# Kernel optimization log

Measured on AMD Instinct MI355X. Metric: run time of the kernel, lower is better.

## Reference

```python
import jax, jax.numpy as jnp
import numpy as np

N = 50000
E = 1600000
D_IN, H1, H2, N_CLS = 512, 128, 64, 10


def _add_self_loops(edge_index, n, edge_attr=None):
    loops = jnp.arange(n, dtype=edge_index.dtype)
    ei = jnp.concatenate([edge_index, jnp.stack([loops, loops])], axis=1)
    if edge_attr is None:
        return ei, None
    # PyG fill_value='mean' for self-loop edge attributes
    loop_attr = jnp.broadcast_to(jnp.mean(edge_attr, axis=0, keepdims=True), (n, edge_attr.shape[1]))
    return ei, jnp.concatenate([edge_attr, loop_attr], axis=0)


def _gat_conv(x, src, dst, n, W, a_src, a_dst, bias, edge_attr=None, We=None, a_edge=None):
    # single-head GATConv
    h = x @ W                                   # (N, out)
    alpha = (h * a_src).sum(-1)[src] + (h * a_dst).sum(-1)[dst]  # (E,)
    if edge_attr is not None:
        alpha = alpha + ((edge_attr @ We) * a_edge).sum(-1)
    alpha = jax.nn.leaky_relu(alpha, 0.2)
    # segment softmax over incoming edges of each dst node
    m = jax.ops.segment_max(alpha, dst, num_segments=n)
    e = jnp.exp(alpha - m[dst])
    s = jax.ops.segment_sum(e, dst, num_segments=n)
    coef = e / (s[dst] + 1e-16)
    out = jax.ops.segment_sum(h[src] * coef[:, None], dst, num_segments=n)
    return out + bias


def _prelu(x, a):
    return jnp.where(x >= 0, x, a * x)


def setup_inputs() -> dict:
    key = jax.random.key(0)
    ks = jax.random.split(key, 24)
    g = lambda k, shape, scale: (jax.random.normal(k, shape, dtype=jnp.float32) * scale)
    inp = {
        "x": jax.random.normal(ks[0], (N, D_IN), dtype=jnp.float32),
        "edge_index": jax.random.randint(ks[1], (2, E), 0, N, dtype=jnp.int32),
        "ppmi_edge_index": jax.random.randint(ks[2], (2, E), 0, N, dtype=jnp.int32),
        "ppmi_edge_attr": jax.random.uniform(ks[3], (E, 1), dtype=jnp.float32),
        # adjacency-branch GAT params
        "W1": g(ks[4], (D_IN, H1), (1.0 / D_IN) ** 0.5),
        "att_src1": g(ks[5], (H1,), 0.1), "att_dst1": g(ks[6], (H1,), 0.1),
        "b1": jnp.zeros((H1,), jnp.float32),
        "W2": g(ks[7], (H1, H2), (1.0 / H1) ** 0.5),
        "att_src2": g(ks[8], (H2,), 0.1), "att_dst2": g(ks[9], (H2,), 0.1),
        "b2": jnp.zeros((H2,), jnp.float32),
        "prelu_a": jnp.float32(0.25),
        # ppmi-branch GAT params (with edge_dim=1)
        "pW1": g(ks[10], (D_IN, H1), (1.0 / D_IN) ** 0.5),
        "patt_src1": g(ks[11], (H1,), 0.1), "patt_dst1": g(ks[12], (H1,), 0.1),
        "pWe1": g(ks[13], (1, H1), 1.0), "patt_e1": g(ks[14], (H1,), 0.1),
        "pb1": jnp.zeros((H1,), jnp.float32),
        "pW2": g(ks[15], (H1, H2), (1.0 / H1) ** 0.5),
        "patt_src2": g(ks[16], (H2,), 0.1), "patt_dst2": g(ks[17], (H2,), 0.1),
        "pWe2": g(ks[18], (1, H2), 1.0), "patt_e2": g(ks[19], (H2,), 0.1),
        "pb2": jnp.zeros((H2,), jnp.float32),
        "pprelu_a": jnp.float32(0.25),
        # fusion attention (Linear(64,1))
        "attn_w": g(ks[20], (H2,), (1.0 / H2) ** 0.5),
        "attn_b": jnp.zeros((), jnp.float32),
        # classifier
        "clf_w": g(ks[21], (H2, N_CLS), (2.0 / H2) ** 0.5),
        "clf_b": jnp.full((N_CLS,), 0.1, jnp.float32),
    }
    return inp


def reference(x, edge_index, ppmi_edge_index, ppmi_edge_attr,
              W1, att_src1, att_dst1, b1, W2, att_src2, att_dst2, b2, prelu_a,
              pW1, patt_src1, patt_dst1, pWe1, patt_e1, pb1,
              pW2, patt_src2, patt_dst2, pWe2, patt_e2, pb2, pprelu_a,
              attn_w, attn_b, clf_w, clf_b):
    n = x.shape[0]
    # adjacency branch (GCN class, GATConv without edge_attr)
    ei, _ = _add_self_loops(edge_index, n)
    src, dst = ei[0], ei[1]
    f1 = _prelu(_gat_conv(x, src, dst, n, W1, att_src1, att_dst1, b1), prelu_a)
    l_out = _prelu(_gat_conv(f1, src, dst, n, W2, att_src2, att_dst2, b2), prelu_a)
    # ppmi branch (GATConv with scalar edge attributes)
    pei, pea = _add_self_loops(ppmi_edge_index, n, ppmi_edge_attr)
    psrc, pdst = pei[0], pei[1]
    g1 = _prelu(_gat_conv(x, psrc, pdst, n, pW1, patt_src1, patt_dst1, pb1, pea, pWe1, patt_e1), pprelu_a)
    g_out = _prelu(_gat_conv(g1, psrc, pdst, n, pW2, patt_src2, patt_dst2, pb2, pea, pWe2, patt_e2), pprelu_a)
    # attn_mode == 1: softmax fusion over stacked branch embeddings
    stacked = jnp.stack([l_out, g_out], axis=1)             # (N, 2, H2)
    scores = stacked @ attn_w + attn_b                      # (N, 2)
    w = jax.nn.softmax(scores, axis=1)[..., None]           # (N, 2, 1)
    emb = jnp.sum(stacked * w, axis=1)                      # (N, H2)
    pred = emb @ clf_w + clf_b                              # (N, n_classes)
    return (emb, pred)
```

## Files before the change

### kernel.cpp

```cpp
#include <hip/hip_runtime.h>


static constexpr int D_IN = 512;
static constexpr int H1c  = 128;
static constexpr int H2c  = 64;
static constexpr int NCLS = 10;

#define DEV __device__ __forceinline__

DEV float waveReduceSum(float v) {
#pragma unroll
  for (int off = 32; off; off >>= 1) v += __shfl_xor(v, off);
  return v;
}

__global__ void k_sum(const float* __restrict__ x, int n, float* __restrict__ out) {
  float v = 0.f;
  for (int i = blockIdx.x * blockDim.x + threadIdx.x; i < n; i += gridDim.x * blockDim.x)
    v += x[i];
  v = waveReduceSum(v);
  if ((threadIdx.x & 63) == 0) atomicAdd(out, v);
}

__global__ void k_edge_coef(const float* __restrict__ We1, const float* __restrict__ ae1,
                            const float* __restrict__ We2, const float* __restrict__ ae2,
                            float* __restrict__ scal) {
  int lane = threadIdx.x;
  float p1 = We1[lane] * ae1[lane] + We1[lane + 64] * ae1[lane + 64];
  float p2 = We2[lane] * ae2[lane];
  p1 = waveReduceSum(p1);
  p2 = waveReduceSum(p2);
  if (lane == 0) { scal[1] = p1; scal[2] = p2; }
}

__global__ void k_count2(const int* __restrict__ eiA, const int* __restrict__ eiP,
                         int E, int n, int* __restrict__ countsA, int* __restrict__ countsP,
                         int* __restrict__ posA, int* __restrict__ posP) {
  int tot = E + n;
  int tot2 = 2 * tot;
  for (int i = blockIdx.x * blockDim.x + threadIdx.x; i < tot2; i += gridDim.x * blockDim.x) {
    bool isP = i >= tot;
    int e = isP ? i - tot : i;
    const int* ei = isP ? eiP : eiA;
    int* counts = isP ? countsP : countsA;
    int* pos = isP ? posP : posA;
    int d = (e < E) ? ei[(size_t)E + e] : (e - E);
    pos[e] = atomicAdd(&counts[d], 1);
  }
}

__global__ void k_scan_block(const int* __restrict__ counts, int n,
                             int* __restrict__ rowptr, int* __restrict__ blockSums) {
  __shared__ int buf[256];
  int tid = threadIdx.x;
  int i = blockIdx.x * 256 + tid;
  int v = (i < n) ? counts[i] : 0;
  buf[tid] = v;
  __syncthreads();
#pragma unroll
  for (int off = 1; off < 256; off <<= 1) {
    int t = (tid >= off) ? buf[tid - off] : 0;
    __syncthreads();
    buf[tid] += t;
    __syncthreads();
  }
  if (i < n) rowptr[i] = buf[tid] - v;
  if (tid == 255) blockSums[blockIdx.x] = buf[255];
}

__global__ void k_scan_sums(int* __restrict__ bs, int nb) {
  __shared__ int buf[256];
  int tid = threadIdx.x;
  int v = (tid < nb) ? bs[tid] : 0;
  buf[tid] = v;
  __syncthreads();
#pragma unroll
  for (int off = 1; off < 256; off <<= 1) {
    int t = (tid >= off) ? buf[tid - off] : 0;
    __syncthreads();
    buf[tid] += t;
    __syncthreads();
  }
  if (tid < nb) bs[tid] = buf[tid] - v;
  if (tid == 255) bs[nb] = buf[255];
}

__global__ void k_scan_add(int* __restrict__ rowptr, const int* __restrict__ bs, int n, int nb) {
  int i = blockIdx.x * blockDim.x + threadIdx.x;
  if (i < n) rowptr[i] += bs[i >> 8];
  else if (i == n) rowptr[n] = bs[nb];
}

__global__ void k_fill2(const int* __restrict__ eiA, const int* __restrict__ eiP,
                        const float* __restrict__ pea, int E, int n,
                        const int* __restrict__ rowptrA, const int* __restrict__ rowptrP,
                        const int* __restrict__ posA, const int* __restrict__ posP,
                        int* __restrict__ srcsA, int2* __restrict__ packP,
                        const float* __restrict__ scal) {
  int tot = E + n;
  int tot2 = 2 * tot;
  float meanea = scal[0] / (float)E;
  for (int i = blockIdx.x * blockDim.x + threadIdx.x; i < tot2; i += gridDim.x * blockDim.x) {
    if (i < tot) {
      int e = i;
      int s, d;
      if (e < E) { s = eiA[e]; d = eiA[(size_t)E + e]; }
      else { s = d = e - E; }
      int slot = rowptrA[d] + posA[e];
      __builtin_nontemporal_store(s, &srcsA[slot]);
    } else {
      int e = i - tot;
      int s, d;
      float ev;
      if (e < E) { s = eiP[e]; d = eiP[(size_t)E + e]; ev = pea[e]; }
      else { s = d = e - E; ev = meanea; }
      int slot = rowptrP[d] + posP[e];
      unsigned long long u =
          ((unsigned long long)__float_as_uint(ev) << 32) | (unsigned int)s;
      __builtin_nontemporal_store(u, (unsigned long long*)&packP[slot]);
    }
  }
}

template <int BM, int BN, int BK, int TM, int TN>
__global__ __launch_bounds__(256) void gemm_f32t_dual(const float* __restrict__ A,
                                                      const float* __restrict__ B1,
                                                      const float* __restrict__ B2,
                                                      float* __restrict__ C1,
                                                      float* __restrict__ C2,
                                                      int M, int N, int K) {
  __shared__ float As[BK][BM + 4];
  __shared__ float B1s[BK][BN + 4];
  __shared__ float B2s[BK][BN + 4];
  constexpr int TX = BN / TN;
  const int tid = threadIdx.x;
  const int tx = tid % TX;
  const int ty = tid / TX;
  const int rowBase = blockIdx.x * BM;
  const int colBase = blockIdx.y * BN;
  float acc1[TM][TN] = {}, acc2[TM][TN] = {};
  constexpr int A4 = (BM * BK / 4) / 256;
  constexpr int B4 = (BN * BK / 4) / 256;
  for (int k0 = 0; k0 < K; k0 += BK) {
#pragma unroll
    for (int it = 0; it < A4; ++it) {
      int idx = it * 256 + tid;
      int row = idx / (BK / 4);
      int cv = (idx % (BK / 4)) * 4;
      int gr = rowBase + row;
      float4 v = make_float4(0.f, 0.f, 0.f, 0.f);
      if (gr < M) v = *(const float4*)(A + (size_t)gr * K + k0 + cv);
      As[cv + 0][row] = v.x;
      As[cv + 1][row] = v.y;
      As[cv + 2][row] = v.z;
      As[cv + 3][row] = v.w;
    }
#pragma unroll
    for (int it = 0; it < B4; ++it) {
      int idx = it * 256 + tid;
      int r = idx / (BN / 4);
      int c = (idx % (BN / 4)) * 4;
      *(float4*)&B1s[r][c] = *(const float4*)(B1 + (size_t)(k0 + r) * N + colBase + c);
      *(float4*)&B2s[r][c] = *(const float4*)(B2 + (size_t)(k0 + r) * N + colBase + c);
    }
    __syncthreads();
#pragma unroll
    for (int kk = 0; kk < BK; ++kk) {
      float a[TM], b1[TN], b2[TN];
#pragma unroll
      for (int i = 0; i < TM; i += 4) *(float4*)&a[i] = *(const float4*)&As[kk][ty * TM + i];
#pragma unroll
      for (int j = 0; j < TN; j += 4) {
        *(float4*)&b1[j] = *(const float4*)&B1s[kk][tx * TN + j];
        *(float4*)&b2[j] = *(const float4*)&B2s[kk][tx * TN + j];
      }
#pragma unroll
      for (int i = 0; i < TM; ++i)
#pragma unroll
        for (int j = 0; j < TN; ++j) {
          acc1[i][j] = fmaf(a[i], b1[j], acc1[i][j]);
          acc2[i][j] = fmaf(a[i], b2[j], acc2[i][j]);
        }
    }
    __syncthreads();
  }
#pragma unroll
  for (int i = 0; i < TM; ++i) {
    int gr = rowBase + ty * TM + i;
    if (gr < M) {
      float* c1p = C1 + (size_t)gr * N + colBase + tx * TN;
      float* c2p = C2 + (size_t)gr * N + colBase + tx * TN;
#pragma unroll
      for (int j = 0; j < TN; j += 4) {
        *(float4*)&c1p[j] = *(const float4*)&acc1[i][j];
        *(float4*)&c2p[j] = *(const float4*)&acc2[i][j];
      }
    }
  }
}

template <int BM, int BN, int BK, int TM, int TN>
__global__ __launch_bounds__(256) void gemm_f32t(const float* __restrict__ A,
                                                 const float* __restrict__ B,
                                                 float* __restrict__ C, int M, int N, int K) {
  __shared__ float As[BK][BM + 4];
  __shared__ float Bs[BK][BN + 4];
  constexpr int TX = BN / TN;
  const int tid = threadIdx.x;
  const int tx = tid % TX;
  const int ty = tid / TX;
  const int rowBase = blockIdx.x * BM;
  const int colBase = blockIdx.y * BN;
  float acc[TM][TN] = {};
  constexpr int A4 = (BM * BK / 4) / 256;
  constexpr int B4 = (BN * BK / 4) / 256;
  for (int k0 = 0; k0 < K; k0 += BK) {
#pragma unroll
    for (int it = 0; it < A4; ++it) {
      int idx = it * 256 + tid;
      int row = idx / (BK / 4);
      int cv = (idx % (BK / 4)) * 4;
      int gr = rowBase + row;
      float4 v = make_float4(0.f, 0.f, 0.f, 0.f);
      if (gr < M) v = *(const float4*)(A + (size_t)gr * K + k0 + cv);
      As[cv + 0][row] = v.x;
      As[cv + 1][row] = v.y;
      As[cv + 2][row] = v.z;
      As[cv + 3][row] = v.w;
    }
#pragma unroll
    for (int it = 0; it < B4; ++it) {
      int idx = it * 256 + tid;
      int r = idx / (BN / 4);
      int c = (idx % (BN / 4)) * 4;
      *(float4*)&Bs[r][c] = *(const float4*)(B + (size_t)(k0 + r) * N + colBase + c);
    }
    __syncthreads();
#pragma unroll
    for (int kk = 0; kk < BK; ++kk) {
      float a[TM], b[TN];
#pragma unroll
      for (int i = 0; i < TM; i += 4) *(float4*)&a[i] = *(const float4*)&As[kk][ty * TM + i];
#pragma unroll
      for (int j = 0; j < TN; j += 4) *(float4*)&b[j] = *(const float4*)&Bs[kk][tx * TN + j];
#pragma unroll
      for (int i = 0; i < TM; ++i)
#pragma unroll
        for (int j = 0; j < TN; ++j) acc[i][j] = fmaf(a[i], b[j], acc[i][j]);
    }
    __syncthreads();
  }
#pragma unroll
  for (int i = 0; i < TM; ++i) {
    int gr = rowBase + ty * TM + i;
    if (gr < M) {
      float* cp = C + (size_t)gr * N + colBase + tx * TN;
#pragma unroll
      for (int j = 0; j < TN; j += 4) *(float4*)&cp[j] = *(const float4*)&acc[i][j];
    }
  }
}

template <int DIM>
__global__ void k_node_dots2(const float* __restrict__ hA, const float* __restrict__ hP,
                             const float* __restrict__ vaA, const float* __restrict__ vbA,
                             const float* __restrict__ vaP, const float* __restrict__ vbP,
                             float* __restrict__ asA, float* __restrict__ adA,
                             float* __restrict__ asP, float* __restrict__ adP, int n) {
  int wid = (blockIdx.x * blockDim.x + threadIdx.x) >> 6;
  int lane = threadIdx.x & 63;
  if (wid >= n) return;
  bool isP = blockIdx.y != 0;
  const float* h = isP ? hP : hA;
  const float* va = isP ? vaP : vaA;
  const float* vb = isP ? vbP : vbA;
  float* oa = isP ? asP : asA;
  float* ob = isP ? adP : adA;
  const float* hr = h + (size_t)wid * DIM;
  float pa = 0.f, pb = 0.f;
#pragma unroll
  for (int v = 0; v < DIM / 64; ++v) {
    float xv = hr[lane + 64 * v];
    pa += xv * va[lane + 64 * v];
    pb += xv * vb[lane + 64 * v];
  }
  pa = waveReduceSum(pa);
  pb = waveReduceSum(pb);
  if (lane == 0) { oa[wid] = pa; ob[wid] = pb; }
}

DEV float leaky02(float a) { return a > 0.f ? a : 0.2f * a; }
DEV float expw(float a) { return __expf(fminf(a, 80.f)); }

template <int DIM>
__global__ void k_gat_agg2(const float* __restrict__ hA, const float* __restrict__ hP,
                           const int* __restrict__ rowptrA, const int* __restrict__ rowptrP,
                           const int* __restrict__ srcsA, const int2* __restrict__ packP,
                           const float* __restrict__ scal, int scal_idx,
                           const float* __restrict__ asA, const float* __restrict__ adA,
                           const float* __restrict__ asP, const float* __restrict__ adP,
                           const float* __restrict__ biasA, const float* __restrict__ biasP,
                           const float* __restrict__ paA, const float* __restrict__ paP,
                           float* __restrict__ outA, float* __restrict__ outP, int n) {
  int wid = (blockIdx.x * blockDim.x + threadIdx.x) >> 6;
  int lane = threadIdx.x & 63;
  if (wid >= n) return;
  bool isP = blockIdx.y != 0;
  const float* h = isP ? hP : hA;
  const int* rowptr = isP ? rowptrP : rowptrA;
  const float* as_ = isP ? asP : asA;
  const float* bias = isP ? biasP : biasA;
  const float* out_ = isP ? outP : outA;
  float adv = (isP ? adP : adA)[wid];
  float pa = (isP ? paP : paA)[0];
  float c = isP ? scal[scal_idx] : 0.f;
  int e0 = rowptr[wid], e1 = rowptr[wid + 1];
  float ssum = 0.f;
  if constexpr (DIM == 128) {
    float2 acc = make_float2(0.f, 0.f);
    int e = e0;
    for (; e + 4 <= e1; e += 4) {
      int s0, s1, s2, s3;
      float a0, a1, a2, a3;
      if (isP) {
        int2 p0 = packP[e], p1 = packP[e + 1], p2 = packP[e + 2], p3 = packP[e + 3];
        s0 = p0.x; s1 = p1.x; s2 = p2.x; s3 = p3.x;
        a0 = c * __int_as_float(p0.y); a1 = c * __int_as_float(p1.y);
        a2 = c * __int_as_float(p2.y); a3 = c * __int_as_float(p3.y);
      } else {
        s0 = srcsA[e]; s1 = srcsA[e + 1]; s2 = srcsA[e + 2]; s3 = srcsA[e + 3];
        a0 = a1 = a2 = a3 = 0.f;
      }
      a0 += as_[s0] + adv; a1 += as_[s1] + adv; a2 += as_[s2] + adv; a3 += as_[s3] + adv;
      float2 h0 = ((const float2*)(h + (size_t)s0 * 128))[lane];
      float2 h1 = ((const float2*)(h + (size_t)s1 * 128))[lane];
      float2 h2 = ((const float2*)(h + (size_t)s2 * 128))[lane];
      float2 h3 = ((const float2*)(h + (size_t)s3 * 128))[lane];
      float w0 = expw(leaky02(a0)), w1 = expw(leaky02(a1));
      float w2 = expw(leaky02(a2)), w3 = expw(leaky02(a3));
      ssum += (w0 + w1) + (w2 + w3);
      acc.x += w0 * h0.x + w1 * h1.x + w2 * h2.x + w3 * h3.x;
      acc.y += w0 * h0.y + w1 * h1.y + w2 * h2.y + w3 * h3.y;
    }
    for (; e < e1; ++e) {
      int s;
      float a;
      if (isP) {
        int2 p = packP[e];
        s = p.x;
        a = c * __int_as_float(p.y);
      } else {
        s = srcsA[e];
        a = 0.f;
      }
      a += as_[s] + adv;
      float w = expw(leaky02(a));
      ssum += w;
      float2 hv = ((const float2*)(h + (size_t)s * 128))[lane];
      acc.x += w * hv.x;
      acc.y += w * hv.y;
    }
    float inv = 1.f / (ssum + 1e-16f);
    float2 bv = ((const float2*)bias)[lane];
    float ox = acc.x * inv + bv.x;
    float oy = acc.y * inv + bv.y;
    ox = ox >= 0.f ? ox : pa * ox;
    oy = oy >= 0.f ? oy : pa * oy;
    ((float2*)((float*)out_ + (size_t)wid * 128))[lane] = make_float2(ox, oy);
  } else {
    float acc = 0.f;
    int e = e0;
    for (; e + 4 <= e1; e += 4) {
      int s0, s1, s2, s3;
      float a0, a1, a2, a3;
      if (isP) {
        int2 p0 = packP[e], p1 = packP[e + 1], p2 = packP[e + 2], p3 = packP[e + 3];
        s0 = p0.x; s1 = p1.x; s2 = p2.x; s3 = p3.x;
        a0 = c * __int_as_float(p0.y); a1 = c * __int_as_float(p1.y);
        a2 = c * __int_as_float(p2.y); a3 = c * __int_as_float(p3.y);
      } else {
        s0 = srcsA[e]; s1 = srcsA[e + 1]; s2 = srcsA[e + 2]; s3 = srcsA[e + 3];
        a0 = a1 = a2 = a3 = 0.f;
      }
      a0 += as_[s0] + adv; a1 += as_[s1] + adv; a2 += as_[s2] + adv; a3 += as_[s3] + adv;
      float h0 = h[(size_t)s0 * 64 + lane];
      float h1 = h[(size_t)s1 * 64 + lane];
      float h2 = h[(size_t)s2 * 64 + lane];
      float h3 = h[(size_t)s3 * 64 + lane];
      float w0 = expw(leaky02(a0)), w1 = expw(leaky02(a1));
      float w2 = expw(leaky02(a2)), w3 = expw(leaky02(a3));
      ssum += (w0 + w1) + (w2 + w3);
      acc += w0 * h0 + w1 * h1 + w2 * h2 + w3 * h3;
    }
    for (; e < e1; ++e) {
      int s;
      float a;
      if (isP) {
        int2 p = packP[e];
        s = p.x;
        a = c * __int_as_float(p.y);
      } else {
        s = srcsA[e];
        a = 0.f;
      }
      a += as_[s] + adv;
      float w = expw(leaky02(a));
      ssum += w;
      acc += w * h[(size_t)s * 64 + lane];
    }
    float inv = 1.f / (ssum + 1e-16f);
    float o = acc * inv + bias[lane];
    o = o >= 0.f ? o : pa * o;
    ((float*)out_)[(size_t)wid * 64 + lane] = o;
  }
}

__global__ void k_fuse(const float* __restrict__ lout, const float* __restrict__ gout,
                       const float* __restrict__ attn_w, const float* __restrict__ attn_b,
                       const float* __restrict__ clf_w, const float* __restrict__ clf_b,
                       float* __restrict__ out, int n) {
  int wid = (blockIdx.x * blockDim.x + threadIdx.x) >> 6;
  int lane = threadIdx.x & 63;
  if (wid >= n) return;
  float l = lout[(size_t)wid * 64 + lane];
  float g = gout[(size_t)wid * 64 + lane];
  float aw = attn_w[lane];
  float s0 = waveReduceSum(l * aw) + attn_b[0];
  float s1 = waveReduceSum(g * aw) + attn_b[0];
  float mx = fmaxf(s0, s1);
  float e0 = __expf(s0 - mx), e1 = __expf(s1 - mx);
  float inv = 1.f / (e0 + e1);
  float w0 = e0 * inv, w1 = e1 * inv;
  float emb = w0 * l + w1 * g;
  out[(size_t)wid * 64 + lane] = emb;
  float p[NCLS];
#pragma unroll
  for (int cc = 0; cc < NCLS; ++cc) p[cc] = emb * clf_w[lane * NCLS + cc];
#pragma unroll
  for (int off = 32; off; off >>= 1)
#pragma unroll
    for (int cc = 0; cc < NCLS; ++cc) p[cc] += __shfl_xor(p[cc], off);
  if (lane < NCLS) {
    float val = 0.f;
#pragma unroll
    for (int cc = 0; cc < NCLS; ++cc)
      if (lane == cc) val = p[cc];
    out[(size_t)n * 64 + (size_t)wid * NCLS + lane] = val + clf_b[lane];
  }
}

extern "C" void kernel_launch(void* const* d_in, const int* in_sizes, int n_in,
                              void* d_out, int out_size, void* d_ws, size_t ws_size,
                              hipStream_t stream) {
  const float* x         = (const float*)d_in[0];
  const int*   ei        = (const int*)d_in[1];
  const int*   pei       = (const int*)d_in[2];
  const float* pea       = (const float*)d_in[3];
  const float* W1        = (const float*)d_in[4];
  const float* att_src1  = (const float*)d_in[5];
  const float* att_dst1  = (const float*)d_in[6];
  const float* b1        = (const float*)d_in[7];
  const float* W2        = (const float*)d_in[8];
  const float* att_src2  = (const float*)d_in[9];
  const float* att_dst2  = (const float*)d_in[10];
  const float* b2        = (const float*)d_in[11];
  const float* prelu_a   = (const float*)d_in[12];
  const float* pW1       = (const float*)d_in[13];
  const float* patt_src1 = (const float*)d_in[14];
  const float* patt_dst1 = (const float*)d_in[15];
  const float* pWe1      = (const float*)d_in[16];
  const float* patt_e1   = (const float*)d_in[17];
  const float* pb1       = (const float*)d_in[18];
  const float* pW2       = (const float*)d_in[19];
  const float* patt_src2 = (const float*)d_in[20];
  const float* patt_dst2 = (const float*)d_in[21];
  const float* pWe2      = (const float*)d_in[22];
  const float* patt_e2   = (const float*)d_in[23];
  const float* pb2       = (const float*)d_in[24];
  const float* pprelu_a  = (const float*)d_in[25];
  const float* attn_w    = (const float*)d_in[26];
  const float* attn_b    = (const float*)d_in[27];
  const float* clf_w     = (const float*)d_in[28];
  const float* clf_b     = (const float*)d_in[29];
  float* out = (float*)d_out;

  const int N = in_sizes[0] / D_IN;
  const int E = in_sizes[1] / 2;
  const int Etot = E + N;

  float* wf = (float*)d_ws;
  size_t o = 0;
  float* h1a = wf + o; o += (size_t)N * H1c;
  float* h1p = wf + o; o += (size_t)N * H1c;
  float* f1a = wf + o; o += (size_t)N * H1c;
  float* g1p = wf + o; o += (size_t)N * H1c;
  float* as_a = wf + o; o += N;
  float* ad_a = wf + o; o += N;
  float* as_p = wf + o; o += N;
  float* ad_p = wf + o; o += N;
  float* scal = wf + o; o += 8;
  float* h2a   = h1a;
  float* l_out = h1a + (size_t)N * H2c;
  float* h2p   = h1p;
  float* g_out = h1p + (size_t)N * H2c;
  int* posA = (int*)f1a;
  int* posP = posA + Etot;

  int* wi = (int*)(wf + o);
  int* rowptrA = wi;
  int* rowptrP = rowptrA + (N + 1);
  int* countsA = rowptrP + (N + 1);
  int* countsP = countsA + N;
  int* blockSums = countsP + N;
  int* srcsA = blockSums + 512;
  int2* packP = (int2*)(srcsA + Etot);
  size_t needBytes = (size_t)((char*)(packP + Etot) - (char*)d_ws);
  if (needBytes > ws_size) return;

  hipMemsetAsync(countsA, 0, sizeof(int) * (size_t)2 * N, stream);
  hipMemsetAsync(scal, 0, sizeof(float) * 8, stream);

  const int GS = 2048;
  k_sum<<<1024, 256, 0, stream>>>(pea, E, scal);
  k_edge_coef<<<1, 64, 0, stream>>>(pWe1, patt_e1, pWe2, patt_e2, scal);

  k_count2<<<GS, 256, 0, stream>>>(ei, pei, E, N, countsA, countsP, posA, posP);
  int nb = (N + 255) / 256;
  int scanAddBlocks = (N + 1 + 255) / 256;
  k_scan_block<<<nb, 256, 0, stream>>>(countsA, N, rowptrA, blockSums);
  k_scan_sums<<<1, 256, 0, stream>>>(blockSums, nb);
  k_scan_add<<<scanAddBlocks, 256, 0, stream>>>(rowptrA, blockSums, N, nb);
  k_scan_block<<<nb, 256, 0, stream>>>(countsP, N, rowptrP, blockSums);
  k_scan_sums<<<1, 256, 0, stream>>>(blockSums, nb);
  k_scan_add<<<scanAddBlocks, 256, 0, stream>>>(rowptrP, blockSums, N, nb);
  k_fill2<<<GS, 256, 0, stream>>>(ei, pei, pea, E, N, rowptrA, rowptrP, posA, posP,
                                  srcsA, packP, scal);

  dim3 g1((N + 127) / 128, H1c / 64);
  gemm_f32t_dual<128, 64, 32, 8, 4><<<g1, 256, 0, stream>>>(x, W1, pW1, h1a, h1p, N, H1c, D_IN);
  int gw = (N + 3) / 4;
  dim3 gd(gw, 2);
  k_node_dots2<H1c><<<gd, 256, 0, stream>>>(h1a, h1p, att_src1, att_dst1, patt_src1,
                                            patt_dst1, as_a, ad_a, as_p, ad_p, N);
  k_gat_agg2<H1c><<<gd, 256, 0, stream>>>(h1a, h1p, rowptrA, rowptrP, srcsA, packP, scal, 1,
                                          as_a, ad_a, as_p, ad_p, b1, pb1, prelu_a, pprelu_a,
                                          f1a, g1p, N);

  dim3 g2((N + 63) / 64, H2c / 64);
  gemm_f32t<64, 64, 32, 4, 4><<<g2, 256, 0, stream>>>(f1a, W2, h2a, N, H2c, H1c);
  gemm_f32t<64, 64, 32, 4, 4><<<g2, 256, 0, stream>>>(g1p, pW2, h2p, N, H2c, H1c);
  k_node_dots2<H2c><<<gd, 256, 0, stream>>>(h2a, h2p, att_src2, att_dst2, patt_src2,
                                            patt_dst2, as_a, ad_a, as_p, ad_p, N);
  k_gat_agg2<H2c><<<gd, 256, 0, stream>>>(h2a, h2p, rowptrA, rowptrP, srcsA, packP, scal, 2,
                                          as_a, ad_a, as_p, ad_p, b2, pb2, prelu_a, pprelu_a,
                                          l_out, g_out, N);

  k_fuse<<<gw, 256, 0, stream>>>(l_out, g_out, attn_w, attn_b, clf_w, clf_b, out, N);
}
```

Measured before the change: 1.171 ms.

## Store GAT node features in fp16 and batch edge weights per wave

```diff
diff --git a/kernel.cpp b/kernel.cpp
--- a/kernel.cpp
+++ b/kernel.cpp
@@ -1,4 +1,5 @@
 #include <hip/hip_runtime.h>
+#include <hip/hip_fp16.h>
 
 
 static constexpr int D_IN = 512;
@@ -123,12 +124,12 @@
 }
 
 template <int BM, int BN, int BK, int TM, int TN>
-__global__ __launch_bounds__(256) void gemm_f32t_dual(const float* __restrict__ A,
-                                                      const float* __restrict__ B1,
-                                                      const float* __restrict__ B2,
-                                                      float* __restrict__ C1,
-                                                      float* __restrict__ C2,
-                                                      int M, int N, int K) {
+__global__ __launch_bounds__(256) void gemm_dual_h(const float* __restrict__ A,
+                                                   const float* __restrict__ B1,
+                                                   const float* __restrict__ B2,
+                                                   __half* __restrict__ C1,
+                                                   __half* __restrict__ C2,
+                                                   int M, int N, int K) {
   __shared__ float As[BK][BM + 4];
   __shared__ float B1s[BK][BN + 4];
   __shared__ float B2s[BK][BN + 4];
@@ -188,21 +189,28 @@
   for (int i = 0; i < TM; ++i) {
     int gr = rowBase + ty * TM + i;
     if (gr < M) {
-      float* c1p = C1 + (size_t)gr * N + colBase + tx * TN;
-      float* c2p = C2 + (size_t)gr * N + colBase + tx * TN;
-#pragma unroll
-      for (int j = 0; j < TN; j += 4) {
-        *(float4*)&c1p[j] = *(const float4*)&acc1[i][j];
-        *(float4*)&c2p[j] = *(const float4*)&acc2[i][j];
+      __half* c1p = C1 + (size_t)gr * N + colBase + tx * TN;
+      __half* c2p = C2 + (size_t)gr * N + colBase + tx * TN;
+#pragma unroll
+      for (int j = 0; j < TN; j += 2) {
+        *(__half2*)&c1p[j] = __floats2half2_rn(acc1[i][j], acc1[i][j + 1]);
+        *(__half2*)&c2p[j] = __floats2half2_rn(acc2[i][j], acc2[i][j + 1]);
       }
     }
   }
 }
 
 template <int BM, int BN, int BK, int TM, int TN>
-__global__ __launch_bounds__(256) void gemm_f32t(const float* __restrict__ A,
-                                                 const float* __restrict__ B,
-                                                 float* __restrict__ C, int M, int N, int K) {
+__global__ __launch_bounds__(256) void gemm_pair_h(const float* __restrict__ A0,
+                                                   const float* __restrict__ A1,
+                                                   const float* __restrict__ B0,
+                                                   const float* __restrict__ B1,
+                                                   __half* __restrict__ C0,
+                                                   __half* __restrict__ C1,
+                                                   int M, int N, int K) {
+  const float* A = blockIdx.z ? A1 : A0;
+  const float* B = blockIdx.z ? B1 : B0;
+  __half* C = blockIdx.z ? C1 : C0;
   __shared__ float As[BK][BM + 4];
   __shared__ float Bs[BK][BN + 4];
   constexpr int TX = BN / TN;
@@ -254,15 +262,16 @@
   for (int i = 0; i < TM; ++i) {
     int gr = rowBase + ty * TM + i;
     if (gr < M) {
-      float* cp = C + (size_t)gr * N + colBase + tx * TN;
-#pragma unroll
-      for (int j = 0; j < TN; j += 4) *(float4*)&cp[j] = *(const float4*)&acc[i][j];
+      __half* cp = C + (size_t)gr * N + colBase + tx * TN;
+#pragma unroll
+      for (int j = 0; j < TN; j += 2)
+        *(__half2*)&cp[j] = __floats2half2_rn(acc[i][j], acc[i][j + 1]);
     }
   }
 }
 
 template <int DIM>
-__global__ void k_node_dots2(const float* __restrict__ hA, const float* __restrict__ hP,
+__global__ void k_node_dots2(const __half* __restrict__ hA, const __half* __restrict__ hP,
                              const float* __restrict__ vaA, const float* __restrict__ vbA,
                              const float* __restrict__ vaP, const float* __restrict__ vbP,
                              float* __restrict__ asA, float* __restrict__ adA,
@@ -271,16 +280,16 @@
   int lane = threadIdx.x & 63;
   if (wid >= n) return;
   bool isP = blockIdx.y != 0;
-  const float* h = isP ? hP : hA;
+  const __half* h = isP ? hP : hA;
   const float* va = isP ? vaP : vaA;
   const float* vb = isP ? vbP : vbA;
   float* oa = isP ? asP : asA;
   float* ob = isP ? adP : adA;
-  const float* hr = h + (size_t)wid * DIM;
+  const __half* hr = h + (size_t)wid * DIM;
   float pa = 0.f, pb = 0.f;
 #pragma unroll
   for (int v = 0; v < DIM / 64; ++v) {
-    float xv = hr[lane + 64 * v];
+    float xv = __half2float(hr[lane + 64 * v]);
     pa += xv * va[lane + 64 * v];
     pb += xv * vb[lane + 64 * v];
   }
@@ -293,7 +302,7 @@
 DEV float expw(float a) { return __expf(fminf(a, 80.f)); }
 
 template <int DIM>
-__global__ void k_gat_agg2(const float* __restrict__ hA, const float* __restrict__ hP,
+__global__ void k_gat_agg2(const __half* __restrict__ hA, const __half* __restrict__ hP,
                            const int* __restrict__ rowptrA, const int* __restrict__ rowptrP,
                            const int* __restrict__ srcsA, const int2* __restrict__ packP,
                            const float* __restrict__ scal, int scal_idx,
@@ -306,112 +315,85 @@
   int lane = threadIdx.x & 63;
   if (wid >= n) return;
   bool isP = blockIdx.y != 0;
-  const float* h = isP ? hP : hA;
+  const char* hb = (const char*)(isP ? hP : hA);
   const int* rowptr = isP ? rowptrP : rowptrA;
   const float* as_ = isP ? asP : asA;
   const float* bias = isP ? biasP : biasA;
-  const float* out_ = isP ? outP : outA;
+  float* outp = isP ? outP : outA;
   float adv = (isP ? adP : adA)[wid];
   float pa = (isP ? paP : paA)[0];
   float c = isP ? scal[scal_idx] : 0.f;
   int e0 = rowptr[wid], e1 = rowptr[wid + 1];
   float ssum = 0.f;
-  if constexpr (DIM == 128) {
-    float2 acc = make_float2(0.f, 0.f);
-    int e = e0;
-    for (; e + 4 <= e1; e += 4) {
-      int s0, s1, s2, s3;
-      float a0, a1, a2, a3;
-      if (isP) {
-        int2 p0 = packP[e], p1 = packP[e + 1], p2 = packP[e + 2], p3 = packP[e + 3];
-        s0 = p0.x; s1 = p1.x; s2 = p2.x; s3 = p3.x;
-        a0 = c * __int_as_float(p0.y); a1 = c * __int_as_float(p1.y);
-        a2 = c * __int_as_float(p2.y); a3 = c * __int_as_float(p3.y);
-      } else {
-        s0 = srcsA[e]; s1 = srcsA[e + 1]; s2 = srcsA[e + 2]; s3 = srcsA[e + 3];
-        a0 = a1 = a2 = a3 = 0.f;
-      }
-      a0 += as_[s0] + adv; a1 += as_[s1] + adv; a2 += as_[s2] + adv; a3 += as_[s3] + adv;
-      float2 h0 = ((const float2*)(h + (size_t)s0 * 128))[lane];
-      float2 h1 = ((const float2*)(h + (size_t)s1 * 128))[lane];
-      float2 h2 = ((const float2*)(h + (size_t)s2 * 128))[lane];
-      float2 h3 = ((const float2*)(h + (size_t)s3 * 128))[lane];
-      float w0 = expw(leaky02(a0)), w1 = expw(leaky02(a1));
-      float w2 = expw(leaky02(a2)), w3 = expw(leaky02(a3));
-      ssum += (w0 + w1) + (w2 + w3);
-      acc.x += w0 * h0.x + w1 * h1.x + w2 * h2.x + w3 * h3.x;
-      acc.y += w0 * h0.y + w1 * h1.y + w2 * h2.y + w3 * h3.y;
-    }
-    for (; e < e1; ++e) {
-      int s;
+  float accx = 0.f, accy = 0.f;
+  const unsigned lb = (DIM == 128) ? ((unsigned)lane << 2) : ((unsigned)lane << 1);
+  for (int base = e0; base < e1; base += 64) {
+    int ee = base + lane;
+    float w = 0.f;
+    int s = 0;
+    if (ee < e1) {
       float a;
       if (isP) {
-        int2 p = packP[e];
+        int2 p = packP[ee];
         s = p.x;
         a = c * __int_as_float(p.y);
       } else {
-        s = srcsA[e];
+        s = srcsA[ee];
         a = 0.f;
       }
       a += as_[s] + adv;
-      float w = expw(leaky02(a));
-      ssum += w;
-      float2 hv = ((const float2*)(h + (size_t)s * 128))[lane];
-      acc.x += w * hv.x;
-      acc.y += w * hv.y;
-    }
-    float inv = 1.f / (ssum + 1e-16f);
+      w = expw(leaky02(a));
+    }
+    ssum += w;
+    int cnt = min(64, e1 - base);
+    int j = 0;
+    for (; j + 4 <= cnt; j += 4) {
+      float w0 = __shfl(w, j), w1 = __shfl(w, j + 1);
+      float w2 = __shfl(w, j + 2), w3 = __shfl(w, j + 3);
+      int s0 = __shfl(s, j), s1 = __shfl(s, j + 1);
+      int s2 = __shfl(s, j + 2), s3 = __shfl(s, j + 3);
+      if constexpr (DIM == 128) {
+        __half2 v0 = *(const __half2*)(hb + (((unsigned)s0 << 8) + lb));
+        __half2 v1 = *(const __half2*)(hb + (((unsigned)s1 << 8) + lb));
+        __half2 v2 = *(const __half2*)(hb + (((unsigned)s2 << 8) + lb));
+        __half2 v3 = *(const __half2*)(hb + (((unsigned)s3 << 8) + lb));
+        float2 f0 = __half22float2(v0), f1 = __half22float2(v1);
+        float2 f2 = __half22float2(v2), f3 = __half22float2(v3);
+        accx += w0 * f0.x + w1 * f1.x + w2 * f2.x + w3 * f3.x;
+        accy += w0 * f0.y + w1 * f1.y + w2 * f2.y + w3 * f3.y;
+      } else {
+        float f0 = __half2float(*(const __half*)(hb + (((unsigned)s0 << 7) + lb)));
+        float f1 = __half2float(*(const __half*)(hb + (((unsigned)s1 << 7) + lb)));
+        float f2 = __half2float(*(const __half*)(hb + (((unsigned)s2 << 7) + lb)));
+        float f3 = __half2float(*(const __half*)(hb + (((unsigned)s3 << 7) + lb)));
+        accx += w0 * f0 + w1 * f1 + w2 * f2 + w3 * f3;
+      }
+    }
+    for (; j < cnt; ++j) {
+      float wj = __shfl(w, j);
+      int sj = __shfl(s, j);
+      if constexpr (DIM == 128) {
+        float2 f = __half22float2(*(const __half2*)(hb + (((unsigned)sj << 8) + lb)));
+        accx += wj * f.x;
+        accy += wj * f.y;
+      } else {
+        accx += wj * __half2float(*(const __half*)(hb + (((unsigned)sj << 7) + lb)));
+      }
+    }
+  }
+  ssum = waveReduceSum(ssum);
+  float inv = 1.f / (ssum + 1e-16f);
+  if constexpr (DIM == 128) {
     float2 bv = ((const float2*)bias)[lane];
-    float ox = acc.x * inv + bv.x;
-    float oy = acc.y * inv + bv.y;
+    float ox = accx * inv + bv.x;
+    float oy = accy * inv + bv.y;
     ox = ox >= 0.f ? ox : pa * ox;
     oy = oy >= 0.f ? oy : pa * oy;
-    ((float2*)((float*)out_ + (size_t)wid * 128))[lane] = make_float2(ox, oy);
+    ((float2*)(outp + (size_t)wid * 128))[lane] = make_float2(ox, oy);
   } else {
-    float acc = 0.f;
-    int e = e0;
-    for (; e + 4 <= e1; e += 4) {
-      int s0, s1, s2, s3;
-      float a0, a1, a2, a3;
-      if (isP) {
-        int2 p0 = packP[e], p1 = packP[e + 1], p2 = packP[e + 2], p3 = packP[e + 3];
-        s0 = p0.x; s1 = p1.x; s2 = p2.x; s3 = p3.x;
-        a0 = c * __int_as_float(p0.y); a1 = c * __int_as_float(p1.y);
-        a2 = c * __int_as_float(p2.y); a3 = c * __int_as_float(p3.y);
-      } else {
-        s0 = srcsA[e]; s1 = srcsA[e + 1]; s2 = srcsA[e + 2]; s3 = srcsA[e + 3];
-        a0 = a1 = a2 = a3 = 0.f;
-      }
-      a0 += as_[s0] + adv; a1 += as_[s1] + adv; a2 += as_[s2] + adv; a3 += as_[s3] + adv;
-      float h0 = h[(size_t)s0 * 64 + lane];
-      float h1 = h[(size_t)s1 * 64 + lane];
-      float h2 = h[(size_t)s2 * 64 + lane];
-      float h3 = h[(size_t)s3 * 64 + lane];
-      float w0 = expw(leaky02(a0)), w1 = expw(leaky02(a1));
-      float w2 = expw(leaky02(a2)), w3 = expw(leaky02(a3));
-      ssum += (w0 + w1) + (w2 + w3);
-      acc += w0 * h0 + w1 * h1 + w2 * h2 + w3 * h3;
-    }
-    for (; e < e1; ++e) {
-      int s;
-      float a;
-      if (isP) {
-        int2 p = packP[e];
-        s = p.x;
-        a = c * __int_as_float(p.y);
-      } else {
-        s = srcsA[e];
-        a = 0.f;
-      }
-      a += as_[s] + adv;
-      float w = expw(leaky02(a));
-      ssum += w;
-      acc += w * h[(size_t)s * 64 + lane];
-    }
-    float inv = 1.f / (ssum + 1e-16f);
-    float o = acc * inv + bias[lane];
+    float o = accx * inv + bias[lane];
     o = o >= 0.f ? o : pa * o;
-    ((float*)out_)[(size_t)wid * 64 + lane] = o;
+    outp[(size_t)wid * 64 + lane] = o;
   }
 }
 
@@ -488,37 +470,40 @@
   const int E = in_sizes[1] / 2;
   const int Etot = E + N;
 
-  float* wf = (float*)d_ws;
-  size_t o = 0;
-  float* h1a = wf + o; o += (size_t)N * H1c;
-  float* h1p = wf + o; o += (size_t)N * H1c;
-  float* f1a = wf + o; o += (size_t)N * H1c;
-  float* g1p = wf + o; o += (size_t)N * H1c;
-  float* as_a = wf + o; o += N;
-  float* ad_a = wf + o; o += N;
-  float* as_p = wf + o; o += N;
-  float* ad_p = wf + o; o += N;
-  float* scal = wf + o; o += 8;
-  float* h2a   = h1a;
-  float* l_out = h1a + (size_t)N * H2c;
-  float* h2p   = h1p;
-  float* g_out = h1p + (size_t)N * H2c;
+  char* wsp = (char*)d_ws;
+  size_t used = 0;
+  auto alloc = [&](size_t bytes) {
+    char* p = wsp + used;
+    used += (bytes + 255) & ~(size_t)255;
+    return p;
+  };
+  __half* h1a_h = (__half*)alloc((size_t)N * H1c * 2);
+  __half* h1p_h = (__half*)alloc((size_t)N * H1c * 2);
+  float*  f1a   = (float*)alloc((size_t)N * H1c * 4);
+  float*  g1p   = (float*)alloc((size_t)N * H1c * 4);
+  __half* h2a_h = (__half*)alloc((size_t)N * H2c * 2);
+  __half* h2p_h = (__half*)alloc((size_t)N * H2c * 2);
+  float*  as_a  = (float*)alloc((size_t)N * 4);
+  float*  ad_a  = (float*)alloc((size_t)N * 4);
+  float*  as_p  = (float*)alloc((size_t)N * 4);
+  float*  ad_p  = (float*)alloc((size_t)N * 4);
+  float*  scal  = (float*)alloc(64);
+  int*    rowptrA = (int*)alloc((size_t)(N + 1) * 4);
+  int*    rowptrP = (int*)alloc((size_t)(N + 1) * 4);
+  int*    countsA = (int*)alloc((size_t)N * 4);
+  int*    countsP = (int*)alloc((size_t)N * 4);
+  int*    blockSums = (int*)alloc(513 * 4);
+  int*    srcsA = (int*)alloc((size_t)Etot * 4);
+  int2*   packP = (int2*)alloc((size_t)Etot * 8);
   int* posA = (int*)f1a;
   int* posP = posA + Etot;
-
-  int* wi = (int*)(wf + o);
-  int* rowptrA = wi;
-  int* rowptrP = rowptrA + (N + 1);
-  int* countsA = rowptrP + (N + 1);
-  int* countsP = countsA + N;
-  int* blockSums = countsP + N;
-  int* srcsA = blockSums + 512;
-  int2* packP = (int2*)(srcsA + Etot);
-  size_t needBytes = (size_t)((char*)(packP + Etot) - (char*)d_ws);
-  if (needBytes > ws_size) return;
-
-  hipMemsetAsync(countsA, 0, sizeof(int) * (size_t)2 * N, stream);
-  hipMemsetAsync(scal, 0, sizeof(float) * 8, stream);
+  float* l_out = (float*)h1a_h;
+  float* g_out = (float*)h1p_h;
+  if (used > ws_size) return;
+
+  hipMemsetAsync(countsA, 0, sizeof(int) * (size_t)N, stream);
+  hipMemsetAsync(countsP, 0, sizeof(int) * (size_t)N, stream);
+  hipMemsetAsync(scal, 0, 64, stream);
 
   const int GS = 2048;
   k_sum<<<1024, 256, 0, stream>>>(pea, E, scal);
@@ -537,23 +522,24 @@
                                   srcsA, packP, scal);
 
   dim3 g1((N + 127) / 128, H1c / 64);
-  gemm_f32t_dual<128, 64, 32, 8, 4><<<g1, 256, 0, stream>>>(x, W1, pW1, h1a, h1p, N, H1c, D_IN);
+  gemm_dual_h<128, 64, 32, 8, 4><<<g1, 256, 0, stream>>>(x, W1, pW1, h1a_h, h1p_h,
+                                                         N, H1c, D_IN);
   int gw = (N + 3) / 4;
   dim3 gd(gw, 2);
-  k_node_dots2<H1c><<<gd, 256, 0, stream>>>(h1a, h1p, att_src1, att_dst1, patt_src1,
+  k_node_dots2<H1c><<<gd, 256, 0, stream>>>(h1a_h, h1p_h, att_src1, att_dst1, patt_src1,
                                             patt_dst1, as_a, ad_a, as_p, ad_p, N);
-  k_gat_agg2<H1c><<<gd, 256, 0, stream>>>(h1a, h1p, rowptrA, rowptrP, srcsA, packP, scal, 1,
-                                          as_a, ad_a, as_p, ad_p, b1, pb1, prelu_a, pprelu_a,
-                                          f1a, g1p, N);
-
-  dim3 g2((N + 63) / 64, H2c / 64);
-  gemm_f32t<64, 64, 32, 4, 4><<<g2, 256, 0, stream>>>(f1a, W2, h2a, N, H2c, H1c);
-  gemm_f32t<64, 64, 32, 4, 4><<<g2, 256, 0, stream>>>(g1p, pW2, h2p, N, H2c, H1c);
-  k_node_dots2<H2c><<<gd, 256, 0, stream>>>(h2a, h2p, att_src2, att_dst2, patt_src2,
+  k_gat_agg2<H1c><<<gd, 256, 0, stream>>>(h1a_h, h1p_h, rowptrA, rowptrP, srcsA, packP,
+                                          scal, 1, as_a, ad_a, as_p, ad_p, b1, pb1,
+                                          prelu_a, pprelu_a, f1a, g1p, N);
+
+  dim3 g2((N + 63) / 64, H2c / 64, 2);
+  gemm_pair_h<64, 64, 32, 4, 4><<<g2, 256, 0, stream>>>(f1a, g1p, W2, pW2, h2a_h, h2p_h,
+                                                        N, H2c, H1c);
+  k_node_dots2<H2c><<<gd, 256, 0, stream>>>(h2a_h, h2p_h, att_src2, att_dst2, patt_src2,
                                             patt_dst2, as_a, ad_a, as_p, ad_p, N);
-  k_gat_agg2<H2c><<<gd, 256, 0, stream>>>(h2a, h2p, rowptrA, rowptrP, srcsA, packP, scal, 2,
-                                          as_a, ad_a, as_p, ad_p, b2, pb2, prelu_a, pprelu_a,
-                                          l_out, g_out, N);
+  k_gat_agg2<H2c><<<gd, 256, 0, stream>>>(h2a_h, h2p_h, rowptrA, rowptrP, srcsA, packP,
+                                          scal, 2, as_a, ad_a, as_p, ad_p, b2, pb2,
+                                          prelu_a, pprelu_a, l_out, g_out, N);
 
   k_fuse<<<gw, 256, 0, stream>>>(l_out, g_out, attn_w, attn_b, clf_w, clf_b, out, N);
 }
```

After: 1.004 ms. 1.17x faster.
